# Kernel optimization log

Hardware: AMD Instinct MI355X
Metric: run time of the kernel (lower is better)

## Reference

```python
import jax, jax.numpy as jnp
import numpy as np

N_NODES = 100000   # num_nodes
N_EDGES = 50000    # num_hyperedges
M = 1600000        # num incidences
D = 64             # hidden_size
N_LAYERS = 1


def setup_inputs() -> dict:
    key = jax.random.key(0)
    k1, k2, k3 = jax.random.split(key, 3)
    x = jax.random.normal(k1, (N_NODES, D), dtype=jnp.float32)
    node_idx = jax.random.randint(k2, (M,), 0, N_NODES, dtype=jnp.int32)
    edge_idx = jax.random.randint(k3, (M,), 0, N_EDGES, dtype=jnp.int32)
    edge_weight = jnp.ones((N_EDGES,), dtype=jnp.float32)
    return {"x": x, "node_idx": node_idx, "edge_idx": edge_idx, "edge_weight": edge_weight}


def _safe_recip(v):
    # 1/v with inf -> 0, matching D[D==inf]=0
    return jnp.where(v > 0, 1.0 / jnp.where(v > 0, v, 1.0), 0.0)


def _hconv(x, node_idx, edge_idx, edge_weight):
    # D[n] = sum over incidences (n,e) of w[e]; B[e] = hyperedge cardinality
    Dn = jax.ops.segment_sum(edge_weight[edge_idx], node_idx, num_segments=N_NODES)
    Dn = _safe_recip(Dn)
    Be = jax.ops.segment_sum(jnp.ones((node_idx.shape[0],), x.dtype), edge_idx, num_segments=N_EDGES)
    Be = _safe_recip(Be)
    # stage 1: nodes -> hyperedges, message = B[e] * x[j]
    edge_feat = jax.ops.segment_sum(x[node_idx] * Be[edge_idx][:, None], edge_idx, num_segments=N_EDGES)
    # stage 2: hyperedges -> nodes, message = D[i] * edge_feat[e]
    out = jax.ops.segment_sum(edge_feat[edge_idx] * Dn[node_idx][:, None], node_idx, num_segments=N_NODES)
    return out


def reference(x, node_idx, edge_idx, edge_weight):
    h = x
    acc = x
    for _ in range(N_LAYERS):
        h = _hconv(h, node_idx, edge_idx, edge_weight)
        acc = acc + h
    return acc / (N_LAYERS + 1)
```

## Files before the change

kernel.cpp:

```cpp
#include <hip/hip_runtime.h>

#define N_NODES 100000
#define N_EDGES 50000
#define N_KEYS  150000
#define M_INC   1600000
#define D_HID   64

#define SUBR    32
#define SUBLEN  50000
#define KPART   8192
#define PN      13
#define PE      7

#define N_TILES_N 25
#define N_TILES_E 13


__device__ __forceinline__ unsigned pack2bf(float a, float b) {
    unsigned ua = __float_as_uint(a); ua = (ua + 0x7fffu + ((ua >> 16) & 1u)) >> 16;
    unsigned ub = __float_as_uint(b); ub = (ub + 0x7fffu + ((ub >> 16) & 1u)) >> 16;
    return ua | (ub << 16);
}

__global__ __launch_bounds__(1024) void count_kernel(
        const int* __restrict__ node_idx, const int* __restrict__ edge_idx,
        unsigned short* __restrict__ rank_n, unsigned short* __restrict__ rank_e,
        unsigned short* __restrict__ cnt_g) {
    __shared__ unsigned int h[KPART];
    int bid = blockIdx.x;
    const int* idx; unsigned short* rk; int p, s, klim, goff;
    if (bid < PN * SUBR) {
        p = bid / SUBR; s = bid % SUBR;
        idx = node_idx; rk = rank_n; klim = N_NODES; goff = 0;
    } else {
        int b2 = bid - PN * SUBR;
        p = b2 / SUBR; s = b2 % SUBR;
        idx = edge_idx; rk = rank_e; klim = N_EDGES; goff = N_NODES;
    }
    int kbase = p * KPART;
    int t = threadIdx.x;
    for (int i = t; i < KPART; i += 1024) h[i] = 0;
    __syncthreads();
    int mbase = s * SUBLEN;
    const int4* src4 = (const int4*)(idx + mbase);
    for (int i = t; i < SUBLEN / 4; i += 1024) {
        int4 v = src4[i];
        int m0 = mbase + i * 4;
        int k;
        k = v.x - kbase; if ((unsigned)k < KPART) rk[m0 + 0] = (unsigned short)atomicAdd(&h[k], 1u);
        k = v.y - kbase; if ((unsigned)k < KPART) rk[m0 + 1] = (unsigned short)atomicAdd(&h[k], 1u);
        k = v.z - kbase; if ((unsigned)k < KPART) rk[m0 + 2] = (unsigned short)atomicAdd(&h[k], 1u);
        k = v.w - kbase; if ((unsigned)k < KPART) rk[m0 + 3] = (unsigned short)atomicAdd(&h[k], 1u);
    }
    __syncthreads();
    for (int i = t; i < KPART; i += 1024) {
        int key = kbase + i;
        if (key < klim) cnt_g[s * N_KEYS + goff + key] = (unsigned short)h[i];
    }
}

__global__ void replprefix_kernel(const unsigned short* __restrict__ cnt_g,
                                  unsigned short* __restrict__ rb, int* __restrict__ tot) {
    int key = blockIdx.x * 256 + threadIdx.x;
    if (key < N_KEYS) {
        int base = 0;
#pragma unroll
        for (int k = 0; k < SUBR; k++) {
            rb[k * N_KEYS + key] = (unsigned short)base;
            base += (int)cnt_g[k * N_KEYS + key];
        }
        tot[key] = base;
    }
}

__global__ void scan_partial_kernel(const int* __restrict__ cnt,
                                    int* __restrict__ pn, int* __restrict__ pe) {
    __shared__ int lds[16];
    int b = blockIdx.x;
    const int* src; int nElem; int tile; int* dst;
    if (b < N_TILES_N) { src = cnt;            nElem = N_NODES; tile = b;             dst = pn; }
    else               { src = cnt + N_NODES;  nElem = N_EDGES; tile = b - N_TILES_N; dst = pe; }
    int t = threadIdx.x;
    int i4 = tile * 1024 + t;
    int sum = 0;
    if (i4 * 4 < nElem) {
        int4 v = ((const int4*)src)[i4];
        sum = v.x + v.y + v.z + v.w;
    }
    for (int off = 1; off < 64; off <<= 1) sum += __shfl_xor(sum, off, 64);
    if ((t & 63) == 0) lds[t >> 6] = sum;
    __syncthreads();
    if (t < 16) {
        int s = lds[t];
        for (int off = 1; off < 16; off <<= 1) s += __shfl_xor(s, off, 64);
        if (t == 0) dst[tile] = s;
    }
}

__global__ void scan_base_kernel(const int* __restrict__ pn, const int* __restrict__ pe,
                                 int* __restrict__ bn, int* __restrict__ be,
                                 int* __restrict__ noff, int* __restrict__ eoff) {
    int w = threadIdx.x >> 6;
    int lane = threadIdx.x & 63;
    if (w == 0) {
        int v = (lane < N_TILES_N) ? pn[lane] : 0;
        int incl = v;
        for (int d = 1; d < 64; d <<= 1) { int u = __shfl_up(incl, d, 64); if (lane >= d) incl += u; }
        if (lane < N_TILES_N) bn[lane] = incl - v;
        if (lane == N_TILES_N - 1) noff[N_NODES] = incl;
    } else {
        int v = (lane < N_TILES_E) ? pe[lane] : 0;
        int incl = v;
        for (int d = 1; d < 64; d <<= 1) { int u = __shfl_up(incl, d, 64); if (lane >= d) incl += u; }
        if (lane < N_TILES_E) be[lane] = incl - v;
        if (lane == N_TILES_E - 1) eoff[N_EDGES] = incl;
    }
}

__global__ void scan_write_kernel(const int* __restrict__ cnt,
                                  const int* __restrict__ bn, const int* __restrict__ be,
                                  int* __restrict__ noff, int* __restrict__ eoff) {
    __shared__ int wsum[16];
    int b = blockIdx.x;
    const int* src; int* dst; int nElem; int tile; int tbase;
    if (b < N_TILES_N) { src = cnt;           dst = noff; nElem = N_NODES; tile = b;             tbase = bn[tile]; }
    else               { src = cnt + N_NODES; dst = eoff; nElem = N_EDGES; tile = b - N_TILES_N; tbase = be[tile]; }
    int t = threadIdx.x;
    int lane = t & 63, w = t >> 6;
    int i4 = tile * 1024 + t;
    int4 c = make_int4(0, 0, 0, 0);
    bool valid = (i4 * 4 < nElem);
    if (valid) c = ((const int4*)src)[i4];
    int tsum = c.x + c.y + c.z + c.w;
    int incl = tsum;
    for (int d = 1; d < 64; d <<= 1) { int u = __shfl_up(incl, d, 64); if (lane >= d) incl += u; }
    if (lane == 63) wsum[w] = incl;
    __syncthreads();
    if (t < 16) {
        int v = wsum[t];
        int wi = v;
        for (int d = 1; d < 16; d <<= 1) { int u = __shfl_up(wi, d, 64); if (t >= d) wi += u; }
        wsum[t] = wi - v;
    }
    __syncthreads();
    int ex = tbase + wsum[w] + incl - tsum;
    if (valid) {
        int4 o;
        o.x = ex; o.y = ex + c.x; o.z = o.y + c.y; o.w = o.z + c.z;
        ((int4*)dst)[i4] = o;
    }
}

__global__ void fill_kernel(const int* __restrict__ node_idx,
                            const int* __restrict__ edge_idx,
                            const unsigned short* __restrict__ rank_n,
                            const unsigned short* __restrict__ rank_e,
                            const unsigned short* __restrict__ rb,
                            const int* __restrict__ noff, const int* __restrict__ eoff,
                            int* __restrict__ node_csr, int* __restrict__ edge_csr) {
    int m = blockIdx.x * 256 + threadIdx.x;
    if (m < M_INC) {
        int s = m / SUBLEN;
        const unsigned short* rbs = rb + s * N_KEYS;
        int n = node_idx[m], e = edge_idx[m];
        node_csr[noff[n] + (int)rbs[n] + (int)rank_n[m]] = e;
        edge_csr[eoff[e] + (int)rbs[N_NODES + e] + (int)rank_e[m]] = n;
    }
}

__global__ void cvt_kernel(const float* __restrict__ x, unsigned int* __restrict__ xh) {
    int i = blockIdx.x * 256 + threadIdx.x;
    if (i < (N_NODES * D_HID) / 8) {
        const float4* x4 = (const float4*)x;
        float4 a = x4[i * 2], b = x4[i * 2 + 1];
        uint4 o;
        o.x = pack2bf(a.x, a.y); o.y = pack2bf(a.z, a.w);
        o.z = pack2bf(b.x, b.y); o.w = pack2bf(b.z, b.w);
        ((uint4*)xh)[i] = o;
    }
}

__global__ void stage1_kernel(const int* __restrict__ eoff, const int* __restrict__ ecsr,
                              const uint4* __restrict__ xh, uint4* __restrict__ ef) {
    int wid = (blockIdx.x * 256 + threadIdx.x) >> 6;
    if (wid >= N_EDGES) return;
    int lane = threadIdx.x & 63;
    int group = lane >> 3;
    int gl = lane & 7;
    int s = eoff[wid], t = eoff[wid + 1];
    float acc[8] = {0.f, 0.f, 0.f, 0.f, 0.f, 0.f, 0.f, 0.f};
    for (int base = s; base < t; base += 64) {
        int idx_l = (base + lane < t) ? ecsr[base + lane] : 0;
        int cnt = t - base; if (cnt > 64) cnt = 64;
        int steps = (cnt + 7) >> 3;
        for (int j = 0; j < steps; j++) {
            int p = 8 * j + group;
            int mi = __shfl(idx_l, p, 64);
            if (p < cnt) {
                uint4 v = xh[(size_t)mi * 8 + gl];
                acc[0] += __uint_as_float(v.x << 16); acc[1] += __uint_as_float(v.x & 0xffff0000u);
                acc[2] += __uint_as_float(v.y << 16); acc[3] += __uint_as_float(v.y & 0xffff0000u);
                acc[4] += __uint_as_float(v.z << 16); acc[5] += __uint_as_float(v.z & 0xffff0000u);
                acc[6] += __uint_as_float(v.w << 16); acc[7] += __uint_as_float(v.w & 0xffff0000u);
            }
        }
    }
    for (int off = 8; off < 64; off <<= 1)
#pragma unroll
        for (int i = 0; i < 8; i++) acc[i] += __shfl_xor(acc[i], off, 64);
    if (group == 0) {
        int card = t - s;
        float ber = (card > 0) ? (1.0f / (float)card) : 0.f;
        uint4 o;
        o.x = pack2bf(acc[0] * ber, acc[1] * ber);
        o.y = pack2bf(acc[2] * ber, acc[3] * ber);
        o.z = pack2bf(acc[4] * ber, acc[5] * ber);
        o.w = pack2bf(acc[6] * ber, acc[7] * ber);
        ef[(size_t)wid * 8 + gl] = o;
    }
}

__global__ void stage2_kernel(const int* __restrict__ noff, const int* __restrict__ ncsr,
                              const uint4* __restrict__ ef, const float* __restrict__ ew,
                              const float* __restrict__ x, float* __restrict__ out) {
    int wid = (blockIdx.x * 256 + threadIdx.x) >> 6;
    if (wid >= N_NODES) return;
    int lane = threadIdx.x & 63;
    int group = lane >> 3;
    int gl = lane & 7;
    int s = noff[wid], t = noff[wid + 1];
    float acc[8] = {0.f, 0.f, 0.f, 0.f, 0.f, 0.f, 0.f, 0.f};
    float dn = 0.f;
    for (int base = s; base < t; base += 64) {
        bool lv = (base + lane < t);
        int idx_l = lv ? ncsr[base + lane] : 0;
        if (lv) dn += ew[idx_l];
        int cnt = t - base; if (cnt > 64) cnt = 64;
        int steps = (cnt + 7) >> 3;
        for (int j = 0; j < steps; j++) {
            int p = 8 * j + group;
            int mi = __shfl(idx_l, p, 64);
            if (p < cnt) {
                uint4 v = ef[(size_t)mi * 8 + gl];
                acc[0] += __uint_as_float(v.x << 16); acc[1] += __uint_as_float(v.x & 0xffff0000u);
                acc[2] += __uint_as_float(v.y << 16); acc[3] += __uint_as_float(v.y & 0xffff0000u);
                acc[4] += __uint_as_float(v.z << 16); acc[5] += __uint_as_float(v.z & 0xffff0000u);
                acc[6] += __uint_as_float(v.w << 16); acc[7] += __uint_as_float(v.w & 0xffff0000u);
            }
        }
    }
    for (int off = 1; off < 64; off <<= 1) dn += __shfl_xor(dn, off, 64);
    for (int off = 8; off < 64; off <<= 1)
#pragma unroll
        for (int i = 0; i < 8; i++) acc[i] += __shfl_xor(acc[i], off, 64);
    if (group == 0) {
        float dnr = (dn > 0.f) ? (1.0f / dn) : 0.f;
        const float4* x4 = (const float4*)x;
        float4* o4 = (float4*)out;
        float4 a = x4[(size_t)wid * 16 + gl * 2];
        float4 b = x4[(size_t)wid * 16 + gl * 2 + 1];
        float4 ra, rb2;
        ra.x = 0.5f * (a.x + dnr * acc[0]);
        ra.y = 0.5f * (a.y + dnr * acc[1]);
        ra.z = 0.5f * (a.z + dnr * acc[2]);
        ra.w = 0.5f * (a.w + dnr * acc[3]);
        rb2.x = 0.5f * (b.x + dnr * acc[4]);
        rb2.y = 0.5f * (b.y + dnr * acc[5]);
        rb2.z = 0.5f * (b.z + dnr * acc[6]);
        rb2.w = 0.5f * (b.w + dnr * acc[7]);
        o4[(size_t)wid * 16 + gl * 2] = ra;
        o4[(size_t)wid * 16 + gl * 2 + 1] = rb2;
    }
}

extern "C" void kernel_launch(void* const* d_in, const int* in_sizes, int n_in,
                              void* d_out, int out_size, void* d_ws, size_t ws_size,
                              hipStream_t stream) {
    const float* x        = (const float*)d_in[0];
    const int*   node_idx = (const int*)d_in[1];
    const int*   edge_idx = (const int*)d_in[2];
    const float* ew       = (const float*)d_in[3];
    float* out = (float*)d_out;

    char* ws = (char*)d_ws;
    unsigned short* rank_n   = (unsigned short*)(ws + 0);
    unsigned short* rank_e   = (unsigned short*)(ws + 3200000);
    int*            noff     = (int*)(ws + 6400000);
    int*            eoff     = (int*)(ws + 6800016);
    int*            node_csr = (int*)(ws + 7000032);
    int*            edge_csr = (int*)(ws + 13400032);
    unsigned short* cnt_g = (unsigned short*)(ws + 7000032);
    unsigned short* rb    = (unsigned short*)(ws + 19800032);
    int*            pn    = (int*)(ws + 29400032);
    int*            pe    = pn + 32;
    int*            bn    = pn + 64;
    int*            be    = pn + 96;
    int*            tot   = (int*)(ws + 29404128);
    unsigned int*   ef    = (unsigned int*)(ws + 0);
    unsigned int*   xh    = (unsigned int*)(ws + 19800032);

    count_kernel<<<(PN + PE) * SUBR, 1024, 0, stream>>>(node_idx, edge_idx, rank_n, rank_e, cnt_g);
    replprefix_kernel<<<(N_KEYS + 255) / 256, 256, 0, stream>>>(cnt_g, rb, tot);
    scan_partial_kernel<<<N_TILES_N + N_TILES_E, 1024, 0, stream>>>(tot, pn, pe);
    scan_base_kernel<<<1, 128, 0, stream>>>(pn, pe, bn, be, noff, eoff);
    scan_write_kernel<<<N_TILES_N + N_TILES_E, 1024, 0, stream>>>(tot, bn, be, noff, eoff);
    fill_kernel<<<(M_INC + 255) / 256, 256, 0, stream>>>(node_idx, edge_idx, rank_n, rank_e,
                                                         rb, noff, eoff, node_csr, edge_csr);
    cvt_kernel<<<((N_NODES * D_HID / 8) + 255) / 256, 256, 0, stream>>>(x, xh);
    stage1_kernel<<<(N_EDGES * 64 + 255) / 256, 256, 0, stream>>>(eoff, edge_csr,
                                                                  (const uint4*)xh, (uint4*)ef);
    stage2_kernel<<<(N_NODES * 64 + 255) / 256, 256, 0, stream>>>(noff, node_csr,
                                                                  (const uint4*)ef, ew, x, out);
}
```

Before: 266.5 us.

## Recompute ranks in fill via LDS atomics, shrink node CSR to u16

```diff
diff --git a/kernel.cpp b/kernel.cpp
--- a/kernel.cpp
+++ b/kernel.cpp
@@ -8,12 +8,15 @@
 
 #define SUBR    32
 #define SUBLEN  50000
-#define KPART   8192
-#define PN      13
-#define PE      7
+#define KPART   16384
+#define PN      7
+#define PE      4
 
 #define N_TILES_N 25
 #define N_TILES_E 13
+
+typedef int   v4i __attribute__((ext_vector_type(4)));
+typedef float v4f __attribute__((ext_vector_type(4)));
 
 
 __device__ __forceinline__ unsigned pack2bf(float a, float b) {
@@ -24,33 +27,30 @@
 
 __global__ __launch_bounds__(1024) void count_kernel(
         const int* __restrict__ node_idx, const int* __restrict__ edge_idx,
-        unsigned short* __restrict__ rank_n, unsigned short* __restrict__ rank_e,
         unsigned short* __restrict__ cnt_g) {
     __shared__ unsigned int h[KPART];
     int bid = blockIdx.x;
-    const int* idx; unsigned short* rk; int p, s, klim, goff;
+    const int* idx; int p, s, klim, goff;
     if (bid < PN * SUBR) {
         p = bid / SUBR; s = bid % SUBR;
-        idx = node_idx; rk = rank_n; klim = N_NODES; goff = 0;
+        idx = node_idx; klim = N_NODES; goff = 0;
     } else {
         int b2 = bid - PN * SUBR;
         p = b2 / SUBR; s = b2 % SUBR;
-        idx = edge_idx; rk = rank_e; klim = N_EDGES; goff = N_NODES;
+        idx = edge_idx; klim = N_EDGES; goff = N_NODES;
     }
     int kbase = p * KPART;
     int t = threadIdx.x;
     for (int i = t; i < KPART; i += 1024) h[i] = 0;
     __syncthreads();
-    int mbase = s * SUBLEN;
-    const int4* src4 = (const int4*)(idx + mbase);
+    const v4i* src4 = (const v4i*)(idx + s * SUBLEN);
     for (int i = t; i < SUBLEN / 4; i += 1024) {
-        int4 v = src4[i];
-        int m0 = mbase + i * 4;
+        v4i v = __builtin_nontemporal_load(&src4[i]);
         int k;
-        k = v.x - kbase; if ((unsigned)k < KPART) rk[m0 + 0] = (unsigned short)atomicAdd(&h[k], 1u);
-        k = v.y - kbase; if ((unsigned)k < KPART) rk[m0 + 1] = (unsigned short)atomicAdd(&h[k], 1u);
-        k = v.z - kbase; if ((unsigned)k < KPART) rk[m0 + 2] = (unsigned short)atomicAdd(&h[k], 1u);
-        k = v.w - kbase; if ((unsigned)k < KPART) rk[m0 + 3] = (unsigned short)atomicAdd(&h[k], 1u);
+        k = v.x - kbase; if ((unsigned)k < KPART) atomicAdd(&h[k], 1u);
+        k = v.y - kbase; if ((unsigned)k < KPART) atomicAdd(&h[k], 1u);
+        k = v.z - kbase; if ((unsigned)k < KPART) atomicAdd(&h[k], 1u);
+        k = v.w - kbase; if ((unsigned)k < KPART) atomicAdd(&h[k], 1u);
     }
     __syncthreads();
     for (int i = t; i < KPART; i += 1024) {
@@ -151,20 +151,51 @@
     }
 }
 
-__global__ void fill_kernel(const int* __restrict__ node_idx,
-                            const int* __restrict__ edge_idx,
-                            const unsigned short* __restrict__ rank_n,
-                            const unsigned short* __restrict__ rank_e,
-                            const unsigned short* __restrict__ rb,
-                            const int* __restrict__ noff, const int* __restrict__ eoff,
-                            int* __restrict__ node_csr, int* __restrict__ edge_csr) {
-    int m = blockIdx.x * 256 + threadIdx.x;
-    if (m < M_INC) {
-        int s = m / SUBLEN;
+__global__ __launch_bounds__(1024) void fill_kernel(
+        const int* __restrict__ node_idx, const int* __restrict__ edge_idx,
+        const unsigned short* __restrict__ rb,
+        const int* __restrict__ noff, const int* __restrict__ eoff,
+        unsigned short* __restrict__ csr_n, unsigned int* __restrict__ csr_e) {
+    __shared__ unsigned int h[KPART];
+    const int part0[8] = {7, 8, 9, 10, 0, 2, 4, 6};
+    const int part1[8] = {-1, -1, -1, -1, 1, 3, 5, -1};
+    int g = blockIdx.x & 7;
+    int j = blockIdx.x >> 3;
+    int p = (j < 32) ? part0[g] : part1[g];
+    if (p < 0) return;
+    int s = j & 31;
+    int t = threadIdx.x;
+    for (int i = t; i < KPART; i += 1024) h[i] = 0;
+    __syncthreads();
+    int mbase = s * SUBLEN;
+    if (p < PN) {
+        int kbase = p * KPART;
+        const v4i* k4 = (const v4i*)(node_idx + mbase);
+        const v4i* v4 = (const v4i*)(edge_idx + mbase);
         const unsigned short* rbs = rb + s * N_KEYS;
-        int n = node_idx[m], e = edge_idx[m];
-        node_csr[noff[n] + (int)rbs[n] + (int)rank_n[m]] = e;
-        edge_csr[eoff[e] + (int)rbs[N_NODES + e] + (int)rank_e[m]] = n;
+        for (int i = t; i < SUBLEN / 4; i += 1024) {
+            v4i kv = __builtin_nontemporal_load(&k4[i]);
+            v4i vv = __builtin_nontemporal_load(&v4[i]);
+            int k;
+            k = kv.x - kbase; if ((unsigned)k < KPART) { unsigned r = atomicAdd(&h[k], 1u); csr_n[noff[kv.x] + (int)rbs[kv.x] + (int)r] = (unsigned short)vv.x; }
+            k = kv.y - kbase; if ((unsigned)k < KPART) { unsigned r = atomicAdd(&h[k], 1u); csr_n[noff[kv.y] + (int)rbs[kv.y] + (int)r] = (unsigned short)vv.y; }
+            k = kv.z - kbase; if ((unsigned)k < KPART) { unsigned r = atomicAdd(&h[k], 1u); csr_n[noff[kv.z] + (int)rbs[kv.z] + (int)r] = (unsigned short)vv.z; }
+            k = kv.w - kbase; if ((unsigned)k < KPART) { unsigned r = atomicAdd(&h[k], 1u); csr_n[noff[kv.w] + (int)rbs[kv.w] + (int)r] = (unsigned short)vv.w; }
+        }
+    } else {
+        int kbase = (p - PN) * KPART;
+        const v4i* k4 = (const v4i*)(edge_idx + mbase);
+        const v4i* v4 = (const v4i*)(node_idx + mbase);
+        const unsigned short* rbs = rb + s * N_KEYS + N_NODES;
+        for (int i = t; i < SUBLEN / 4; i += 1024) {
+            v4i kv = __builtin_nontemporal_load(&k4[i]);
+            v4i vv = __builtin_nontemporal_load(&v4[i]);
+            int k;
+            k = kv.x - kbase; if ((unsigned)k < KPART) { unsigned r = atomicAdd(&h[k], 1u); csr_e[eoff[kv.x] + (int)rbs[kv.x] + (int)r] = (unsigned)vv.x; }
+            k = kv.y - kbase; if ((unsigned)k < KPART) { unsigned r = atomicAdd(&h[k], 1u); csr_e[eoff[kv.y] + (int)rbs[kv.y] + (int)r] = (unsigned)vv.y; }
+            k = kv.z - kbase; if ((unsigned)k < KPART) { unsigned r = atomicAdd(&h[k], 1u); csr_e[eoff[kv.z] + (int)rbs[kv.z] + (int)r] = (unsigned)vv.z; }
+            k = kv.w - kbase; if ((unsigned)k < KPART) { unsigned r = atomicAdd(&h[k], 1u); csr_e[eoff[kv.w] + (int)rbs[kv.w] + (int)r] = (unsigned)vv.w; }
+        }
     }
 }
 
@@ -180,7 +211,7 @@
     }
 }
 
-__global__ void stage1_kernel(const int* __restrict__ eoff, const int* __restrict__ ecsr,
+__global__ void stage1_kernel(const int* __restrict__ eoff, const unsigned int* __restrict__ ecsr,
                               const uint4* __restrict__ xh, uint4* __restrict__ ef) {
     int wid = (blockIdx.x * 256 + threadIdx.x) >> 6;
     if (wid >= N_EDGES) return;
@@ -190,13 +221,13 @@
     int s = eoff[wid], t = eoff[wid + 1];
     float acc[8] = {0.f, 0.f, 0.f, 0.f, 0.f, 0.f, 0.f, 0.f};
     for (int base = s; base < t; base += 64) {
-        int idx_l = (base + lane < t) ? ecsr[base + lane] : 0;
+        int idx_l = (base + lane < t) ? (int)__builtin_nontemporal_load(&ecsr[base + lane]) : 0;
         int cnt = t - base; if (cnt > 64) cnt = 64;
         int steps = (cnt + 7) >> 3;
         for (int j = 0; j < steps; j++) {
-            int p = 8 * j + group;
-            int mi = __shfl(idx_l, p, 64);
-            if (p < cnt) {
+            int pp = 8 * j + group;
+            int mi = __shfl(idx_l, pp, 64);
+            if (pp < cnt) {
                 uint4 v = xh[(size_t)mi * 8 + gl];
                 acc[0] += __uint_as_float(v.x << 16); acc[1] += __uint_as_float(v.x & 0xffff0000u);
                 acc[2] += __uint_as_float(v.y << 16); acc[3] += __uint_as_float(v.y & 0xffff0000u);
@@ -220,7 +251,7 @@
     }
 }
 
-__global__ void stage2_kernel(const int* __restrict__ noff, const int* __restrict__ ncsr,
+__global__ void stage2_kernel(const int* __restrict__ noff, const unsigned short* __restrict__ ncsr,
                               const uint4* __restrict__ ef, const float* __restrict__ ew,
                               const float* __restrict__ x, float* __restrict__ out) {
     int wid = (blockIdx.x * 256 + threadIdx.x) >> 6;
@@ -233,14 +264,14 @@
     float dn = 0.f;
     for (int base = s; base < t; base += 64) {
         bool lv = (base + lane < t);
-        int idx_l = lv ? ncsr[base + lane] : 0;
+        int idx_l = lv ? (int)__builtin_nontemporal_load(&ncsr[base + lane]) : 0;
         if (lv) dn += ew[idx_l];
         int cnt = t - base; if (cnt > 64) cnt = 64;
         int steps = (cnt + 7) >> 3;
         for (int j = 0; j < steps; j++) {
-            int p = 8 * j + group;
-            int mi = __shfl(idx_l, p, 64);
-            if (p < cnt) {
+            int pp = 8 * j + group;
+            int mi = __shfl(idx_l, pp, 64);
+            if (pp < cnt) {
                 uint4 v = ef[(size_t)mi * 8 + gl];
                 acc[0] += __uint_as_float(v.x << 16); acc[1] += __uint_as_float(v.x & 0xffff0000u);
                 acc[2] += __uint_as_float(v.y << 16); acc[3] += __uint_as_float(v.y & 0xffff0000u);
@@ -256,10 +287,9 @@
     if (group == 0) {
         float dnr = (dn > 0.f) ? (1.0f / dn) : 0.f;
         const float4* x4 = (const float4*)x;
-        float4* o4 = (float4*)out;
         float4 a = x4[(size_t)wid * 16 + gl * 2];
         float4 b = x4[(size_t)wid * 16 + gl * 2 + 1];
-        float4 ra, rb2;
+        v4f ra, rb2;
         ra.x = 0.5f * (a.x + dnr * acc[0]);
         ra.y = 0.5f * (a.y + dnr * acc[1]);
         ra.z = 0.5f * (a.z + dnr * acc[2]);
@@ -268,8 +298,8 @@
         rb2.y = 0.5f * (b.y + dnr * acc[5]);
         rb2.z = 0.5f * (b.z + dnr * acc[6]);
         rb2.w = 0.5f * (b.w + dnr * acc[7]);
-        o4[(size_t)wid * 16 + gl * 2] = ra;
-        o4[(size_t)wid * 16 + gl * 2 + 1] = rb2;
+        __builtin_nontemporal_store(ra, &((v4f*)out)[(size_t)wid * 16 + gl * 2]);
+        __builtin_nontemporal_store(rb2, &((v4f*)out)[(size_t)wid * 16 + gl * 2 + 1]);
     }
 }
 
@@ -283,32 +313,29 @@
     float* out = (float*)d_out;
 
     char* ws = (char*)d_ws;
-    unsigned short* rank_n   = (unsigned short*)(ws + 0);
-    unsigned short* rank_e   = (unsigned short*)(ws + 3200000);
-    int*            noff     = (int*)(ws + 6400000);
-    int*            eoff     = (int*)(ws + 6800016);
-    int*            node_csr = (int*)(ws + 7000032);
-    int*            edge_csr = (int*)(ws + 13400032);
-    unsigned short* cnt_g = (unsigned short*)(ws + 7000032);
-    unsigned short* rb    = (unsigned short*)(ws + 19800032);
-    int*            pn    = (int*)(ws + 29400032);
+    int*            noff  = (int*)(ws + 0);
+    int*            eoff  = (int*)(ws + 400016);
+    unsigned short* csr_n = (unsigned short*)(ws + 600032);
+    unsigned int*   csr_e = (unsigned int*)(ws + 3800032);
+    unsigned int*   ef    = (unsigned int*)(ws + 10200032);
+    unsigned int*   xh    = (unsigned int*)(ws + 16600032);
+    unsigned short* cnt_g = (unsigned short*)(ws + 600032);
+    unsigned short* rb    = (unsigned short*)(ws + 16600032);
+    int*            tot   = (int*)(ws + 26200032);
+    int*            pn    = (int*)(ws + 26800032);
     int*            pe    = pn + 32;
     int*            bn    = pn + 64;
     int*            be    = pn + 96;
-    int*            tot   = (int*)(ws + 29404128);
-    unsigned int*   ef    = (unsigned int*)(ws + 0);
-    unsigned int*   xh    = (unsigned int*)(ws + 19800032);
-
-    count_kernel<<<(PN + PE) * SUBR, 1024, 0, stream>>>(node_idx, edge_idx, rank_n, rank_e, cnt_g);
+
+    count_kernel<<<(PN + PE) * SUBR, 1024, 0, stream>>>(node_idx, edge_idx, cnt_g);
     replprefix_kernel<<<(N_KEYS + 255) / 256, 256, 0, stream>>>(cnt_g, rb, tot);
     scan_partial_kernel<<<N_TILES_N + N_TILES_E, 1024, 0, stream>>>(tot, pn, pe);
     scan_base_kernel<<<1, 128, 0, stream>>>(pn, pe, bn, be, noff, eoff);
     scan_write_kernel<<<N_TILES_N + N_TILES_E, 1024, 0, stream>>>(tot, bn, be, noff, eoff);
-    fill_kernel<<<(M_INC + 255) / 256, 256, 0, stream>>>(node_idx, edge_idx, rank_n, rank_e,
-                                                         rb, noff, eoff, node_csr, edge_csr);
+    fill_kernel<<<512, 1024, 0, stream>>>(node_idx, edge_idx, rb, noff, eoff, csr_n, csr_e);
     cvt_kernel<<<((N_NODES * D_HID / 8) + 255) / 256, 256, 0, stream>>>(x, xh);
-    stage1_kernel<<<(N_EDGES * 64 + 255) / 256, 256, 0, stream>>>(eoff, edge_csr,
+    stage1_kernel<<<(N_EDGES * 64 + 255) / 256, 256, 0, stream>>>(eoff, csr_e,
                                                                   (const uint4*)xh, (uint4*)ef);
-    stage2_kernel<<<(N_NODES * 64 + 255) / 256, 256, 0, stream>>>(noff, node_csr,
+    stage2_kernel<<<(N_NODES * 64 + 255) / 256, 256, 0, stream>>>(noff, csr_n,
                                                                   (const uint4*)ef, ew, x, out);
 }
```

After: 326.0 us. +22.3%, slower.
